# Kernel optimization log

Hardware: AMD Instinct MI355X
Metric: run time of the kernel (lower is better)

Reference implementation:

```python
import jax, jax.numpy as jnp
import numpy as np

B, S, D = 4, 2048, 1024

def setup_inputs() -> dict:
    key = jax.random.key(0)
    kx, kk, kq, kv = jax.random.split(key, 4)
    scale = 1.0 / np.sqrt(D)
    x = jax.random.normal(kx, (B, S, D), dtype=jnp.float32)
    # nn.Linear weights, applied as x @ W.T; init with small scale like torch default
    Wk = jax.random.normal(kk, (D, D), dtype=jnp.float32) * scale
    Wq = jax.random.normal(kq, (D, D), dtype=jnp.float32) * scale
    Wv = jax.random.normal(kv, (D, D), dtype=jnp.float32) * scale
    return {"x": x, "Wk": Wk, "Wq": Wq, "Wv": Wv}

def reference(x, Wk, Wq, Wv):
    # k/q/v: (B, S, D) @ (D, D_out) -- Linear applies W as x @ W.T
    k = jnp.einsum('bsd,kd->bsk', x, Wk)
    q = jnp.einsum('bsd,kd->bsk', x, Wq)
    v = jnp.einsum('bsd,vd->bsv', x, Wv)
    # scaled dot-product scores: (B, S, S)
    scores = jnp.einsum('bqk,bsk->bqs', q, k) / jnp.sqrt(jnp.asarray(k.shape[-1], x.dtype))
    # causal mask: allow j <= i (upper-right masked out)
    S_len = x.shape[1]
    causal = jnp.tril(jnp.ones((S_len, S_len), dtype=bool))
    scores = jnp.where(causal[None, :, :], scores, jnp.asarray(-jnp.inf, x.dtype))
    weights = jax.nn.softmax(scores, axis=-1)
    # dropout is identity in eval / p used as deterministic baseline
    out = jnp.einsum('bqs,bsv->bqv', weights, v)
    return out
```

## Files before the change

kernel.cpp:

```cpp
#include <hip/hip_runtime.h>

typedef __attribute__((ext_vector_type(8))) short bf16x8;
typedef __attribute__((ext_vector_type(4))) float f32x4;
typedef __attribute__((ext_vector_type(4))) unsigned short u16x4;
typedef __attribute__((ext_vector_type(8))) unsigned short u16x8;

#define MFMA16(a, b, c) __builtin_amdgcn_mfma_f32_16x16x32_bf16((a), (b), (c), 0, 0, 0)

__device__ __forceinline__ ushort f2bf(float f) {
    unsigned u = __float_as_uint(f);
    unsigned r = (u + 0x7FFFu + ((u >> 16) & 1u)) >> 16;
    return (ushort)r;
}
__device__ __forceinline__ float bf2f(ushort s) {
    return __uint_as_float(((unsigned)s) << 16);
}

__device__ __forceinline__ void async16(const ushort* g, ushort* l) {
    __builtin_amdgcn_global_load_lds(
        (const __attribute__((address_space(1))) unsigned*)g,
        (__attribute__((address_space(3))) unsigned*)l, 16, 0, 0);
}

#define SBAR()  __builtin_amdgcn_s_barrier()
#define SCHED() __builtin_amdgcn_sched_barrier(0)

__global__ __launch_bounds__(256) void cvt_all(
    const float* __restrict__ x,  const float* __restrict__ wk,
    const float* __restrict__ wq, const float* __restrict__ wv,
    ushort* __restrict__ xb,  ushort* __restrict__ wvb,
    ushort* __restrict__ wkt, ushort* __restrict__ wqt)
{
    __shared__ float t[32][33];
    int bx = blockIdx.x;
    if (bx < 4608) {
        const size_t XN = (size_t)8192 * 1024;
        size_t idx = ((size_t)bx * 256 + threadIdx.x) * 8;
        const float* s;
        ushort* d;
        if (idx < XN) { s = x + idx; d = xb + idx; }
        else          { s = wv + (idx - XN); d = wvb + (idx - XN); }
        float4 a = *(const float4*)s;
        float4 b = *(const float4*)(s + 4);
        u16x8 p;
        p[0] = f2bf(a.x); p[1] = f2bf(a.y); p[2] = f2bf(a.z); p[3] = f2bf(a.w);
        p[4] = f2bf(b.x); p[5] = f2bf(b.y); p[6] = f2bf(b.z); p[7] = f2bf(b.w);
        *(u16x8*)d = p;
    } else {
        bx -= 4608;
        const int z  = bx >> 10;
        const int tb = bx & 1023;
        const int e0 = (tb & 31) * 32, d0 = (tb >> 5) * 32;
        const float* src = z ? wq : wk;
        ushort*      dst = z ? wqt : wkt;
        const int tx = threadIdx.x & 31, ty = threadIdx.x >> 5;
#pragma unroll
        for (int r = 0; r < 4; ++r)
            t[ty + 8 * r][tx] = src[(size_t)(e0 + ty + 8 * r) * 1024 + d0 + tx];
        __syncthreads();
#pragma unroll
        for (int r = 0; r < 4; ++r)
            dst[(size_t)(d0 + ty + 8 * r) * 1024 + e0 + tx] = f2bf(t[tx][ty + 8 * r]);
    }
}

__device__ __forceinline__ void mma_tile(
    const ushort* __restrict__ A, int lda, int abase,
    const ushort* __restrict__ B, int ldb, int bbase,
    int ktiles,
    ushort* As, ushort* Bs, f32x4 (&acc)[4][4])
{
    const int tid  = threadIdx.x;
    const int lane = tid & 63, wid = tid >> 6;
    const int wr = wid >> 1, wc = wid & 1;
    const int lrow = lane & 15, kgrp = lane >> 4;
    const int ci = lane >> 3;
    const int cc = (lane & 7) * 8;

#pragma unroll
    for (int m = 0; m < 4; ++m)
#pragma unroll
        for (int n = 0; n < 4; ++n) acc[m][n] = (f32x4){0.f, 0.f, 0.f, 0.f};

    for (int kt = 0; kt < ktiles; ++kt) {
        const int k0 = kt * 64;
#pragma unroll
        for (int i = 0; i < 4; ++i) {
            const int r = (wid * 4 + i) * 8 + ci;
            async16(&A[(size_t)(abase + r) * lda + k0 + cc], &As[(wid * 4 + i) * 512]);
            async16(&B[(size_t)(bbase + r) * ldb + k0 + cc], &Bs[(wid * 4 + i) * 512]);
        }
        __syncthreads();
#pragma unroll
        for (int kk = 0; kk < 2; ++kk) {
            bf16x8 af[4], bfr[4];
#pragma unroll
            for (int m = 0; m < 4; ++m)
                af[m] = *(const bf16x8*)&As[(wr * 64 + m * 16 + lrow) * 64 + kk * 32 + kgrp * 8];
#pragma unroll
            for (int n = 0; n < 4; ++n)
                bfr[n] = *(const bf16x8*)&Bs[(wc * 64 + n * 16 + lrow) * 64 + kk * 32 + kgrp * 8];
#pragma unroll
            for (int m = 0; m < 4; ++m)
#pragma unroll
                for (int n = 0; n < 4; ++n)
                    acc[m][n] = MFMA16(af[m], bfr[n], acc[m][n]);
        }
        __syncthreads();
    }
}

__device__ __forceinline__ void mma256(
    const ushort* __restrict__ A, int lda, int abase,
    const ushort* __restrict__ B, int ldb, int bbase,
    int NT, ushort* As, ushort* Bs, f32x4 (&acc)[8][4])
{
    const int tid  = threadIdx.x;
    const int lane = tid & 63, w = tid >> 6;
    const int wr = w >> 2, wc = w & 3;
    const int lrow = lane & 15, kgrp = lane >> 4;
    const int sgl  = ((lane & 7) ^ ((lane >> 3) & 7)) * 8;
    const int srow = lane >> 3;

    auto stage = [&](int t, int isB, int hi) {
        const ushort* src = isB ? B : A;
        const int ld = isB ? ldb : lda;
        const int rb = isB ? bbase : abase;
        ushort* buf = (isB ? Bs : As) + (size_t)(t & 1) * 16384;
#pragma unroll
        for (int i = 0; i < 2; ++i) {
            const int r = hi * 128 + (w * 2 + i) * 8 + srow;
            async16(&src[(size_t)(rb + r) * ld + t * 64 + sgl],
                    buf + (size_t)(hi * 128 + (w * 2 + i) * 8) * 64 + lane * 8);
        }
    };

#pragma unroll
    for (int m = 0; m < 8; ++m)
#pragma unroll
        for (int n = 0; n < 4; ++n) acc[m][n] = (f32x4){0.f, 0.f, 0.f, 0.f};

    stage(0, 0, 0); stage(0, 0, 1); stage(0, 1, 0); stage(0, 1, 1);
    if (NT > 1) {
        stage(1, 0, 0); stage(1, 0, 1);
        asm volatile("s_waitcnt vmcnt(4)" ::: "memory");
    } else {
        asm volatile("s_waitcnt vmcnt(0)" ::: "memory");
    }
    SCHED();
    SBAR();
    SCHED();

    const int sw = lrow & 7;

    for (int t = 0; t < NT; ++t) {
        ushort* Ab = As + (size_t)(t & 1) * 16384;
        ushort* Bb = Bs + (size_t)(t & 1) * 16384;
        bf16x8 af[8], bfr[2];

        {
            const int g = (kgrp ^ sw) * 8;
#pragma unroll
            for (int m = 0; m < 8; ++m)
                af[m] = *(const bf16x8*)&Ab[(wr * 128 + m * 16 + lrow) * 64 + g];
#pragma unroll
            for (int n = 0; n < 2; ++n)
                bfr[n] = *(const bf16x8*)&Bb[(wc * 64 + n * 16 + lrow) * 64 + g];
        }
        if (t + 1 < NT) stage(t + 1, 1, 0);
        SBAR(); SCHED();
        __builtin_amdgcn_s_setprio(1);
#pragma unroll
        for (int m = 0; m < 8; ++m) {
            acc[m][0] = MFMA16(af[m], bfr[0], acc[m][0]);
            acc[m][1] = MFMA16(af[m], bfr[1], acc[m][1]);
        }
        __builtin_amdgcn_s_setprio(0);
        SBAR(); SCHED();

        {
            const int g = (kgrp ^ sw) * 8;
#pragma unroll
            for (int n = 0; n < 2; ++n)
                bfr[n] = *(const bf16x8*)&Bb[(wc * 64 + (2 + n) * 16 + lrow) * 64 + g];
        }
        if (t + 1 < NT) stage(t + 1, 1, 1);
        SBAR(); SCHED();
        __builtin_amdgcn_s_setprio(1);
#pragma unroll
        for (int m = 0; m < 8; ++m) {
            acc[m][2] = MFMA16(af[m], bfr[0], acc[m][2]);
            acc[m][3] = MFMA16(af[m], bfr[1], acc[m][3]);
        }
        __builtin_amdgcn_s_setprio(0);
        SBAR(); SCHED();

        {
            const int g = ((4 + kgrp) ^ sw) * 8;
#pragma unroll
            for (int m = 0; m < 8; ++m)
                af[m] = *(const bf16x8*)&Ab[(wr * 128 + m * 16 + lrow) * 64 + g];
#pragma unroll
            for (int n = 0; n < 2; ++n)
                bfr[n] = *(const bf16x8*)&Bb[(wc * 64 + n * 16 + lrow) * 64 + g];
        }
        SBAR(); SCHED();
        __builtin_amdgcn_s_setprio(1);
#pragma unroll
        for (int m = 0; m < 8; ++m) {
            acc[m][0] = MFMA16(af[m], bfr[0], acc[m][0]);
            acc[m][1] = MFMA16(af[m], bfr[1], acc[m][1]);
        }
        __builtin_amdgcn_s_setprio(0);
        SBAR(); SCHED();

        {
            const int g = ((4 + kgrp) ^ sw) * 8;
#pragma unroll
            for (int n = 0; n < 2; ++n)
                bfr[n] = *(const bf16x8*)&Bb[(wc * 64 + (2 + n) * 16 + lrow) * 64 + g];
        }
        if (t + 2 < NT) {
            stage(t + 2, 0, 0); stage(t + 2, 0, 1);
            asm volatile("s_waitcnt vmcnt(4)" ::: "memory");
        } else if (t + 1 < NT) {
            asm volatile("s_waitcnt vmcnt(0)" ::: "memory");
        }
        SCHED();
        SBAR(); SCHED();
        __builtin_amdgcn_s_setprio(1);
#pragma unroll
        for (int m = 0; m < 8; ++m) {
            acc[m][2] = MFMA16(af[m], bfr[0], acc[m][2]);
            acc[m][3] = MFMA16(af[m], bfr[1], acc[m][3]);
        }
        __builtin_amdgcn_s_setprio(0);
        SBAR(); SCHED();
    }
}

__global__ __launch_bounds__(256) void m_gemm(
    const ushort* __restrict__ Wkt, const ushort* __restrict__ Wqt,
    ushort* __restrict__ Mtr)
{
    __shared__ ushort As[128 * 64];
    __shared__ ushort Bs[128 * 64];
    const int fbase = blockIdx.x * 128;
    const int dbase = blockIdx.y * 128;

    f32x4 acc[4][4];
    mma_tile(Wkt, 1024, fbase, Wqt, 1024, dbase, 16, As, Bs, acc);

    const int lane = threadIdx.x & 63, wid = threadIdx.x >> 6;
    const int wr = wid >> 1, wc = wid & 1;
    const int lrow = lane & 15, kgrp = lane >> 4;
#pragma unroll
    for (int m = 0; m < 4; ++m)
#pragma unroll
        for (int n = 0; n < 4; ++n)
#pragma unroll
            for (int r = 0; r < 4; ++r) {
                const int gf = fbase + wr * 64 + m * 16 + kgrp * 4 + r;
                const int gd = dbase + wc * 64 + n * 16 + lrow;
                Mtr[(size_t)gf * 1024 + gd] = f2bf(acc[m][n][r] * 0.03125f);
            }
}

__global__ __launch_bounds__(512, 2) void tv_gemm8(
    const ushort* __restrict__ xb, const ushort* __restrict__ Mtr,
    const ushort* __restrict__ Wvb,
    ushort* __restrict__ Tb, ushort* __restrict__ Vt)
{
    __shared__ ushort As[2 * 16384];
    __shared__ ushort Bs[2 * 16384];

    const int z = blockIdx.z;
    const ushort* Bmat = z ? Wvb : Mtr;
    const int mbase = blockIdx.x * 256;
    const int nbase = blockIdx.y * 256;

    f32x4 acc[8][4];
    mma256(xb, 1024, mbase, Bmat, 1024, nbase, 16, As, Bs, acc);

    const int lane = threadIdx.x & 63, w = threadIdx.x >> 6;
    const int wr = w >> 2, wc = w & 3;
    const int lrow = lane & 15, kgrp = lane >> 4;

    if (z == 1) {
        const int b  = mbase >> 11;
        const int s0 = mbase & 2047;
        ushort* VtB = Vt + (size_t)b * 1024 * 2048;
#pragma unroll
        for (int m = 0; m < 8; ++m)
#pragma unroll
            for (int n = 0; n < 4; ++n) {
                u16x4 pk;
#pragma unroll
                for (int r = 0; r < 4; ++r) pk[r] = f2bf(acc[m][n][r]);
                const int d = nbase + wc * 64 + n * 16 + lrow;
                const int s = s0 + wr * 128 + m * 16 + kgrp * 4;
                *(u16x4*)&VtB[(size_t)d * 2048 + s] = pk;
            }
    } else {
#pragma unroll
        for (int m = 0; m < 8; ++m)
#pragma unroll
            for (int n = 0; n < 4; ++n)
#pragma unroll
                for (int r = 0; r < 4; ++r) {
                    const int gr = mbase + wr * 128 + m * 16 + kgrp * 4 + r;
                    const int gc = nbase + wc * 64 + n * 16 + lrow;
                    Tb[(size_t)gr * 1024 + gc] = f2bf(acc[m][n][r]);
                }
    }
}

__global__ __launch_bounds__(512, 2) void scores_gemm8(
    const ushort* __restrict__ Tb, const ushort* __restrict__ xb,
    ushort* __restrict__ Sall, float* __restrict__ rsum)
{
    __shared__ ushort As[2 * 16384];
    __shared__ ushort Bs[2 * 16384];

    ushort* S = Sall + (size_t)blockIdx.y * 2048 * 2048;
    const int rb = blockIdx.y * 2048;

    int t = blockIdx.x;
    int it = (int)((sqrtf(8.0f * (float)t + 1.0f) - 1.0f) * 0.5f);
    while ((it + 1) * (it + 2) / 2 <= t) ++it;
    while (it * (it + 1) / 2 > t) --it;
    const int jt = t - it * (it + 1) / 2;
    const int ibase = it * 256, jbase = jt * 256;
    const bool diag = (it == jt);

    f32x4 acc[8][4];
    mma256(Tb, 1024, rb + ibase, xb, 1024, rb + jbase, 16, As, Bs, acc);

    const int tid = threadIdx.x;
    const int lane = tid & 63, w = tid >> 6;
    const int wr = w >> 2, wc = w & 3;
    const int lrow = lane & 15, kgrp = lane >> 4;

    float prs[8][4];
#pragma unroll
    for (int m = 0; m < 8; ++m)
#pragma unroll
        for (int r = 0; r < 4; ++r) prs[m][r] = 0.f;

#pragma unroll
    for (int m = 0; m < 8; ++m)
#pragma unroll
        for (int n = 0; n < 4; ++n)
#pragma unroll
            for (int r = 0; r < 4; ++r) {
                const int gi = ibase + wr * 128 + m * 16 + kgrp * 4 + r;
                const int gj = jbase + wc * 64 + n * 16 + lrow;
                float p = __expf(acc[m][n][r]);
                if (diag && gj > gi) p = 0.f;
                S[(size_t)gi * 2048 + gj] = f2bf(p);
                prs[m][r] += p;
            }

    float* psum = (float*)As;
#pragma unroll
    for (int m = 0; m < 8; ++m)
#pragma unroll
        for (int r = 0; r < 4; ++r) {
            float v = prs[m][r];
            v += __shfl_xor(v, 1);
            v += __shfl_xor(v, 2);
            v += __shfl_xor(v, 4);
            v += __shfl_xor(v, 8);
            prs[m][r] = v;
        }
    if (lrow == 0) {
#pragma unroll
        for (int m = 0; m < 8; ++m)
#pragma unroll
            for (int r = 0; r < 4; ++r)
                psum[(wr * 4 + wc) * 128 + m * 16 + kgrp * 4 + r] = prs[m][r];
    }
    __syncthreads();
    if (tid < 256) {
        const int half = tid >> 7, rr = tid & 127;
        float s4 = psum[(half * 4 + 0) * 128 + rr] + psum[(half * 4 + 1) * 128 + rr]
                 + psum[(half * 4 + 2) * 128 + rr] + psum[(half * 4 + 3) * 128 + rr];
        rsum[(size_t)(blockIdx.y * 9 + jt) * 2048 + ibase + tid] = s4;
    }
}

__device__ __forceinline__ void pv_sub(
    const ushort* __restrict__ P, const ushort* __restrict__ Vt,
    float* __restrict__ O, const float* __restrict__ rsb,
    int it, int nbase, ushort* As, ushort* Bs, float* rs)
{
    const int tid  = threadIdx.x;
    const int lane = tid & 63, w = tid >> 6;
    const int wr = w >> 2, wc = w & 3;
    const int lrow = lane & 15, kgrp = lane >> 4;
    const int srow = lane >> 3;
    const int sc16 = (lane & 7) ^ srow;
    const int pbase = it * 128;
    const int NT = 2 * (it + 1);
    const int jtmax = it >> 1;

    auto stage = [&](int t, int slot) {
        ushort* dA = As + (size_t)slot * 8192;
        ushort* dB = Bs + (size_t)slot * 8192;
#pragma unroll
        for (int i = 0; i < 2; ++i) {
            const int rr = (i * 8 + w) * 8 + srow;
            async16(&P [(size_t)(pbase + rr) * 2048 + t * 64 + sc16 * 8],
                    dA + ((i * 8 + w) * 64 + lane) * 8);
            async16(&Vt[(size_t)(nbase + rr) * 2048 + t * 64 + sc16 * 8],
                    dB + ((i * 8 + w) * 64 + lane) * 8);
        }
    };

    if (tid < 128) {
        float s = 0.f;
        for (int j = 0; j <= jtmax; ++j)
            s += rsb[(size_t)j * 2048 + pbase + tid];
        rs[tid] = 1.0f / s;
    }

    f32x4 acc[4][2];
#pragma unroll
    for (int m = 0; m < 4; ++m)
#pragma unroll
        for (int n = 0; n < 2; ++n) acc[m][n] = (f32x4){0.f, 0.f, 0.f, 0.f};

    stage(0, 0);
    if (NT > 2) {
        stage(1, 1); stage(2, 2);
        asm volatile("s_waitcnt vmcnt(8)" ::: "memory");
    } else {
        stage(1, 1);
        asm volatile("s_waitcnt vmcnt(4)" ::: "memory");
    }
    SCHED();
    SBAR(); SCHED();

    int bi = 0;
    for (int t = 0; t < NT; ++t) {
        const ushort* Ab = As + (size_t)bi * 8192;
        const ushort* Bb = Bs + (size_t)bi * 8192;
        bf16x8 af[2][4], bq[2][2];
#pragma unroll
        for (int kk = 0; kk < 2; ++kk) {
            const int p16 = (kk * 4 + kgrp) ^ (lrow & 7);
#pragma unroll
            for (int m = 0; m < 4; ++m) {
                const int row = wr * 64 + m * 16 + lrow;
                af[kk][m] = *(const bf16x8*)&Ab[row * 64 + p16 * 8];
            }
#pragma unroll
            for (int n = 0; n < 2; ++n) {
                const int row = wc * 32 + n * 16 + lrow;
                bq[kk][n] = *(const bf16x8*)&Bb[row * 64 + p16 * 8];
            }
        }
        asm volatile("s_waitcnt lgkmcnt(0)" ::: "memory");
        SCHED();
        SBAR(); SCHED();
        if (t + 3 < NT) {
            stage(t + 3, bi);
            asm volatile("s_waitcnt vmcnt(8)" ::: "memory");
        } else if (t + 3 == NT) {
            asm volatile("s_waitcnt vmcnt(4)" ::: "memory");
        } else if (t + 2 == NT) {
            asm volatile("s_waitcnt vmcnt(0)" ::: "memory");
        }
        SCHED();
        SBAR(); SCHED();
        __builtin_amdgcn_s_setprio(1);
#pragma unroll
        for (int kk = 0; kk < 2; ++kk)
#pragma unroll
            for (int m = 0; m < 4; ++m) {
                acc[m][0] = MFMA16(af[kk][m], bq[kk][0], acc[m][0]);
                acc[m][1] = MFMA16(af[kk][m], bq[kk][1], acc[m][1]);
            }
        __builtin_amdgcn_s_setprio(0);
        bi = (bi == 2) ? 0 : bi + 1;
    }

    __syncthreads();

#pragma unroll
    for (int m = 0; m < 4; ++m)
#pragma unroll
        for (int r = 0; r < 4; ++r) {
            const int ri = wr * 64 + m * 16 + kgrp * 4 + r;
            const float inv = rs[ri];
            const int gi = pbase + ri;
#pragma unroll
            for (int n = 0; n < 2; ++n) {
                const int gc = nbase + wc * 32 + n * 16 + lrow;
                O[(size_t)gi * 1024 + gc] = acc[m][n][r] * inv;
            }
        }
    __syncthreads();
}

__global__ __launch_bounds__(512, 2) void pv_pair(
    const ushort* __restrict__ Pall, const ushort* __restrict__ Vtall,
    const float* __restrict__ rsum, float* __restrict__ Oall)
{
    __shared__ ushort As[3 * 8192];
    __shared__ ushort Bs[3 * 8192];
    __shared__ float rs[128];

    const ushort* P  = Pall  + (size_t)blockIdx.z * 2048 * 2048;
    const ushort* Vt = Vtall + (size_t)blockIdx.z * 1024 * 2048;
    const float* rsb = rsum  + (size_t)blockIdx.z * 9 * 2048;
    float*        O  = Oall  + (size_t)blockIdx.z * 2048 * 1024;
    const int nbase = blockIdx.y * 128;

    pv_sub(P, Vt, O, rsb, 15 - (int)blockIdx.x, nbase, As, Bs, rs);
    pv_sub(P, Vt, O, rsb, (int)blockIdx.x,      nbase, As, Bs, rs);
}

extern "C" void kernel_launch(void* const* d_in, const int* in_sizes, int n_in,
                              void* d_out, int out_size, void* d_ws, size_t ws_size,
                              hipStream_t stream)
{
    (void)in_sizes; (void)n_in; (void)out_size; (void)ws_size;
    const float* x  = (const float*)d_in[0];
    const float* Wk = (const float*)d_in[1];
    const float* Wq = (const float*)d_in[2];
    const float* Wv = (const float*)d_in[3];
    float* out = (float*)d_out;

    const size_t M1 = (size_t)1024 * 1024;
    ushort* ws  = (ushort*)d_ws;
    ushort* xb  = ws;
    ushort* Tb  = xb  + 8 * M1;
    ushort* Vt  = Tb  + 8 * M1;
    ushort* Sb  = Vt  + 8 * M1;
    ushort* Wkt = Sb  + 16 * M1;
    ushort* Wqt = Wkt + M1;
    ushort* Wvb = Wqt + M1;
    ushort* Mtr = Wvb + M1;
    float*  rsum = (float*)(Mtr + M1);

    cvt_all<<<6656, 256, 0, stream>>>(x, Wk, Wq, Wv, xb, Wvb, Wkt, Wqt);
    m_gemm<<<dim3(8, 8), 256, 0, stream>>>(Wkt, Wqt, Mtr);
    tv_gemm8<<<dim3(32, 4, 2), 512, 0, stream>>>(xb, Mtr, Wvb, Tb, Vt);
    scores_gemm8<<<dim3(36, 4), 512, 0, stream>>>(Tb, xb, Sb, rsum);
    pv_pair<<<dim3(8, 8, 4), 512, 0, stream>>>(Sb, Vt, rsum, out);
}
```

Baseline: 149.2 us.

## Split LDS stage buffers into k-halves to issue global prefetches earlier

The shared GEMM mainloop now lays out each 64-wide K tile in LDS as two 32-wide halves with a 4-group XOR swizzle, where before it used one 64-wide row with an 8-group swizzle. Prefetches are issued per half: the next tile's B half-1 plus two halves of the tile after it, spread across the four MFMA phases, with waits set to vmcnt(6). The goal is to spread global-to-LDS traffic more evenly across compute phases and keep more loads in flight. The risks are more bank conflicts from the narrower swizzle and ordering errors in the finer-grained wait counts.

```diff
diff --git a/kernel.cpp b/kernel.cpp
--- a/kernel.cpp
+++ b/kernel.cpp
@@ -119,19 +119,19 @@
     const int lane = tid & 63, w = tid >> 6;
     const int wr = w >> 2, wc = w & 3;
     const int lrow = lane & 15, kgrp = lane >> 4;
-    const int sgl  = ((lane & 7) ^ ((lane >> 3) & 7)) * 8;
-    const int srow = lane >> 3;
-
-    auto stage = [&](int t, int isB, int hi) {
+
+    auto stage = [&](int t, int isB, int kk) {
         const ushort* src = isB ? B : A;
         const int ld = isB ? ldb : lda;
         const int rb = isB ? bbase : abase;
-        ushort* buf = (isB ? Bs : As) + (size_t)(t & 1) * 16384;
+        ushort* slot = (isB ? Bs : As) + (size_t)((t & 1) * 2 + kk) * 8192;
 #pragma unroll
         for (int i = 0; i < 2; ++i) {
-            const int r = hi * 128 + (w * 2 + i) * 8 + srow;
-            async16(&src[(size_t)(rb + r) * ld + t * 64 + sgl],
-                    buf + (size_t)(hi * 128 + (w * 2 + i) * 8) * 64 + lane * 8);
+            const int G = (w * 2 + i) * 64 + lane;
+            const int r = G >> 2, g = G & 3;
+            const int sg = g ^ ((r >> 2) & 3);
+            async16(&src[(size_t)(rb + r) * ld + t * 64 + kk * 32 + sg * 8],
+                    slot + (size_t)G * 8);
         }
     };
 
@@ -140,10 +140,10 @@
 #pragma unroll
         for (int n = 0; n < 4; ++n) acc[m][n] = (f32x4){0.f, 0.f, 0.f, 0.f};
 
-    stage(0, 0, 0); stage(0, 0, 1); stage(0, 1, 0); stage(0, 1, 1);
+    stage(0, 0, 0); stage(0, 1, 0); stage(0, 0, 1); stage(0, 1, 1);
     if (NT > 1) {
-        stage(1, 0, 0); stage(1, 0, 1);
-        asm volatile("s_waitcnt vmcnt(4)" ::: "memory");
+        stage(1, 0, 0); stage(1, 1, 0); stage(1, 0, 1);
+        asm volatile("s_waitcnt vmcnt(6)" ::: "memory");
     } else {
         asm volatile("s_waitcnt vmcnt(0)" ::: "memory");
     }
@@ -151,23 +151,22 @@
     SBAR();
     SCHED();
 
-    const int sw = lrow & 7;
+    const int pg = (kgrp ^ ((lrow >> 2) & 3)) * 8;
 
     for (int t = 0; t < NT; ++t) {
-        ushort* Ab = As + (size_t)(t & 1) * 16384;
-        ushort* Bb = Bs + (size_t)(t & 1) * 16384;
+        ushort* A0 = As + (size_t)((t & 1) * 2 + 0) * 8192;
+        ushort* A1 = As + (size_t)((t & 1) * 2 + 1) * 8192;
+        ushort* B0 = Bs + (size_t)((t & 1) * 2 + 0) * 8192;
+        ushort* B1 = Bs + (size_t)((t & 1) * 2 + 1) * 8192;
         bf16x8 af[8], bfr[2];
 
-        {
-            const int g = (kgrp ^ sw) * 8;
-#pragma unroll
-            for (int m = 0; m < 8; ++m)
-                af[m] = *(const bf16x8*)&Ab[(wr * 128 + m * 16 + lrow) * 64 + g];
-#pragma unroll
-            for (int n = 0; n < 2; ++n)
-                bfr[n] = *(const bf16x8*)&Bb[(wc * 64 + n * 16 + lrow) * 64 + g];
-        }
-        if (t + 1 < NT) stage(t + 1, 1, 0);
+#pragma unroll
+        for (int m = 0; m < 8; ++m)
+            af[m] = *(const bf16x8*)&A0[(wr * 128 + m * 16 + lrow) * 32 + pg];
+#pragma unroll
+        for (int n = 0; n < 2; ++n)
+            bfr[n] = *(const bf16x8*)&B0[(wc * 64 + n * 16 + lrow) * 32 + pg];
+        if (t + 1 < NT) stage(t + 1, 1, 1);
         SBAR(); SCHED();
         __builtin_amdgcn_s_setprio(1);
 #pragma unroll
@@ -178,13 +177,10 @@
         __builtin_amdgcn_s_setprio(0);
         SBAR(); SCHED();
 
-        {
-            const int g = (kgrp ^ sw) * 8;
-#pragma unroll
-            for (int n = 0; n < 2; ++n)
-                bfr[n] = *(const bf16x8*)&Bb[(wc * 64 + (2 + n) * 16 + lrow) * 64 + g];
-        }
-        if (t + 1 < NT) stage(t + 1, 1, 1);
+#pragma unroll
+        for (int n = 0; n < 2; ++n)
+            bfr[n] = *(const bf16x8*)&B0[(wc * 64 + (2 + n) * 16 + lrow) * 32 + pg];
+        if (t + 2 < NT) stage(t + 2, 0, 0);
         SBAR(); SCHED();
         __builtin_amdgcn_s_setprio(1);
 #pragma unroll
@@ -195,15 +191,13 @@
         __builtin_amdgcn_s_setprio(0);
         SBAR(); SCHED();
 
-        {
-            const int g = ((4 + kgrp) ^ sw) * 8;
-#pragma unroll
-            for (int m = 0; m < 8; ++m)
-                af[m] = *(const bf16x8*)&Ab[(wr * 128 + m * 16 + lrow) * 64 + g];
-#pragma unroll
-            for (int n = 0; n < 2; ++n)
-                bfr[n] = *(const bf16x8*)&Bb[(wc * 64 + n * 16 + lrow) * 64 + g];
-        }
+#pragma unroll
+        for (int m = 0; m < 8; ++m)
+            af[m] = *(const bf16x8*)&A1[(wr * 128 + m * 16 + lrow) * 32 + pg];
+#pragma unroll
+        for (int n = 0; n < 2; ++n)
+            bfr[n] = *(const bf16x8*)&B1[(wc * 64 + n * 16 + lrow) * 32 + pg];
+        if (t + 2 < NT) stage(t + 2, 1, 0);
         SBAR(); SCHED();
         __builtin_amdgcn_s_setprio(1);
 #pragma unroll
@@ -214,15 +208,12 @@
         __builtin_amdgcn_s_setprio(0);
         SBAR(); SCHED();
 
-        {
-            const int g = ((4 + kgrp) ^ sw) * 8;
-#pragma unroll
-            for (int n = 0; n < 2; ++n)
-                bfr[n] = *(const bf16x8*)&Bb[(wc * 64 + (2 + n) * 16 + lrow) * 64 + g];
-        }
+#pragma unroll
+        for (int n = 0; n < 2; ++n)
+            bfr[n] = *(const bf16x8*)&B1[(wc * 64 + (2 + n) * 16 + lrow) * 32 + pg];
         if (t + 2 < NT) {
-            stage(t + 2, 0, 0); stage(t + 2, 0, 1);
-            asm volatile("s_waitcnt vmcnt(4)" ::: "memory");
+            stage(t + 2, 0, 1);
+            asm volatile("s_waitcnt vmcnt(6)" ::: "memory");
         } else if (t + 1 < NT) {
             asm volatile("s_waitcnt vmcnt(0)" ::: "memory");
         }
@@ -271,8 +262,8 @@
     const ushort* __restrict__ Wvb,
     ushort* __restrict__ Tb, ushort* __restrict__ Vt)
 {
-    __shared__ ushort As[2 * 16384];
-    __shared__ ushort Bs[2 * 16384];
+    __shared__ ushort As[4 * 8192];
+    __shared__ ushort Bs[4 * 8192];
 
     const int z = blockIdx.z;
     const ushort* Bmat = z ? Wvb : Mtr;
@@ -319,8 +310,8 @@
     const ushort* __restrict__ Tb, const ushort* __restrict__ xb,
     ushort* __restrict__ Sall, float* __restrict__ rsum)
 {
-    __shared__ ushort As[2 * 16384];
-    __shared__ ushort Bs[2 * 16384];
+    __shared__ ushort As[4 * 8192];
+    __shared__ ushort Bs[4 * 8192];
 
     ushort* S = Sall + (size_t)blockIdx.y * 2048 * 2048;
     const int rb = blockIdx.y * 2048;
```

After: 170.0 us. +13.9%, slower.
